# Optimization experiments

Measured on AMD Instinct MI355X. Metric: run time of the kernel, lower is better.

## Reference

```python
import jax, jax.numpy as jnp
import numpy as np

N_NODES = 100000
N_EDGES = 1600000
D_IN = 128
D_HID = 128


def setup_inputs() -> dict:
    key = jax.random.key(0)
    ks = jax.random.split(key, 8)
    scale_in = 1.0 / np.sqrt(D_IN)
    scale_h = 1.0 / np.sqrt(D_HID)
    return {
        "x": jax.random.normal(ks[0], (N_NODES, D_IN), dtype=jnp.float32),
        "edge_index": jax.random.randint(ks[1], (2, N_EDGES), 0, N_NODES, dtype=jnp.int64),
        "W_l1": jax.random.normal(ks[2], (D_IN, D_HID), dtype=jnp.float32) * scale_in,
        "W_r1": jax.random.normal(ks[3], (D_IN, D_HID), dtype=jnp.float32) * scale_in,
        "b1": jnp.zeros((D_HID,), dtype=jnp.float32),
        "W_l2": jax.random.normal(ks[4], (D_HID, D_HID), dtype=jnp.float32) * scale_h,
        "W_r2": jax.random.normal(ks[5], (D_HID, D_HID), dtype=jnp.float32) * scale_h,
        "b2": jnp.zeros((D_HID,), dtype=jnp.float32),
    }


def _sage_conv(h, src, dst, n_nodes, W_l, W_r, b):
    # mean aggregation of source-node features onto destination nodes
    msg = h[src]                                         # [E, d] gather
    agg = jax.ops.segment_sum(msg, dst, num_segments=n_nodes)   # [N, d]
    cnt = jax.ops.segment_sum(jnp.ones((src.shape[0], 1), h.dtype), dst,
                              num_segments=n_nodes)      # [N, 1]
    mean = agg / jnp.maximum(cnt, 1.0)                   # zero where no in-edges
    return mean @ W_l + b + h @ W_r                      # lin_l(mean) + lin_r(x)


def reference(x, edge_index, W_l1, W_r1, b1, W_l2, W_r2, b2):
    src, dst = edge_index[0], edge_index[1]
    n = x.shape[0]
    h = jax.nn.relu(_sage_conv(x, src, dst, n, W_l1, W_r1, b1))
    # dropout is identity in eval mode
    return _sage_conv(h, src, dst, n, W_l2, W_r2, b2)
```

## Files before the change

### kernel.cpp

```cpp
#include <hip/hip_runtime.h>
#include <stdint.h>

#define N_NODES 100000
#define N_EDGES 1600000
#define D 128
#define NBUCK 196
#define BSTRIDE 9216
#define PCHUNK 4096
#define NTILES (N_NODES / 16)
#define GRID_AG 2048

typedef unsigned int uint32;
typedef __attribute__((ext_vector_type(8))) short short8;
typedef __attribute__((ext_vector_type(4))) float f32x4;

__device__ __forceinline__ unsigned short f2bf(float f) {
  unsigned u = __builtin_bit_cast(unsigned, f);
  u += 0x7fffu + ((u >> 16) & 1u);
  return (unsigned short)(u >> 16);
}
__device__ __forceinline__ float bflo(unsigned v) {
  return __builtin_bit_cast(float, v << 16);
}
__device__ __forceinline__ float bfhi(unsigned v) {
  return __builtin_bit_cast(float, v & 0xffff0000u);
}


__global__ void k_zero(int* __restrict__ p, int n) {
  int i = blockIdx.x * blockDim.x + threadIdx.x;
  if (i < n) p[i] = 0;
}

__global__ __launch_bounds__(256) void k_part(const int* __restrict__ src,
                                              const int* __restrict__ dst,
                                              int* __restrict__ bcnt,
                                              uint2* __restrict__ pairs) {
  __shared__ uint2 buff[PCHUNK];
  __shared__ uint2 sorted[PCHUNK];
  __shared__ int hist[256], stmp[256], loff[256], cpos[256], base[256];
  int tid = threadIdx.x;
  int e0 = blockIdx.x * PCHUNK;
  int nv = N_EDGES - e0;
  if (nv > PCHUNK) nv = PCHUNK;

  hist[tid] = 0;
  __syncthreads();
  for (int i = tid; i < nv; i += 256) {
    int d = dst[e0 + i];
    int s = src[e0 + i];
    buff[i] = make_uint2((uint32)d, (uint32)s);
    atomicAdd(&hist[d >> 9], 1);
  }
  __syncthreads();
  int v = hist[tid];
  stmp[tid] = v;
  __syncthreads();
  for (int off = 1; off < 256; off <<= 1) {
    int t = (tid >= off) ? stmp[tid - off] : 0;
    __syncthreads();
    stmp[tid] += t;
    __syncthreads();
  }
  loff[tid] = stmp[tid] - v;
  cpos[tid] = stmp[tid] - v;
  base[tid] = (v > 0) ? atomicAdd(&bcnt[tid], v) : 0;
  __syncthreads();
  for (int i = tid; i < nv; i += 256) {
    uint2 p = buff[i];
    int r = atomicAdd(&cpos[p.x >> 9], 1);
    sorted[r] = p;
  }
  __syncthreads();
  for (int i = tid; i < nv; i += 256) {
    uint2 p = sorted[i];
    int b = (int)(p.x >> 9);
    int local = base[b] + (i - loff[b]);
    if (local < BSTRIDE)
      pairs[(size_t)b * BSTRIDE + local] = p;
  }
}

__global__ void k_scanb(const int* __restrict__ bcnt, int* __restrict__ bbase) {
  __shared__ int s[256];
  int tid = threadIdx.x;
  int v = (tid < NBUCK) ? bcnt[tid] : 0;
  s[tid] = v;
  __syncthreads();
  for (int off = 1; off < 256; off <<= 1) {
    int t = (tid >= off) ? s[tid - off] : 0;
    __syncthreads();
    s[tid] += t;
    __syncthreads();
  }
  if (tid <= NBUCK) bbase[tid] = s[tid] - v;
}

__global__ __launch_bounds__(512) void k_csr(const uint2* __restrict__ pairs,
                                             const int* __restrict__ bcnt,
                                             const int* __restrict__ bbase,
                                             int* __restrict__ rowptr,
                                             int* __restrict__ csr) {
  __shared__ int hist[512], off[512], cur[512];
  int b = blockIdx.x;
  int tid = threadIdx.x;
  int lo = b << 9;
  int hi = lo + 512;
  if (hi > N_NODES) hi = N_NODES;
  int ne = bcnt[b];
  if (ne > BSTRIDE) ne = BSTRIDE;
  const uint2* pb = pairs + (size_t)b * BSTRIDE;
  int bb = bbase[b];

  hist[tid] = 0;
  __syncthreads();
  for (int i = tid; i < ne; i += 512) atomicAdd(&hist[(int)pb[i].x - lo], 1);
  __syncthreads();
  int v = hist[tid];
  off[tid] = v;
  __syncthreads();
  for (int o = 1; o < 512; o <<= 1) {
    int t = (tid >= o) ? off[tid - o] : 0;
    __syncthreads();
    off[tid] += t;
    __syncthreads();
  }
  off[tid] -= v;
  cur[tid] = off[tid];
  if (lo + tid < hi) rowptr[lo + tid] = bb + off[tid];
  if (b == NBUCK - 1 && tid == 0) rowptr[N_NODES] = bbase[NBUCK];
  __syncthreads();
  for (int i = tid; i < ne; i += 512) {
    int d = (int)pb[i].x - lo;
    int slot = atomicAdd(&cur[d], 1);
    csr[bb + slot] = (int)pb[i].y;
  }
}


__global__ void k_cast(const float* __restrict__ in, unsigned short* __restrict__ ob, int n8) {
  int i = blockIdx.x * blockDim.x + threadIdx.x;
  if (i >= n8) return;
  float4 a = *reinterpret_cast<const float4*>(in + (size_t)i * 8);
  float4 b = *reinterpret_cast<const float4*>(in + (size_t)i * 8 + 4);
  uint4 o;
  o.x = (uint32)f2bf(a.x) | ((uint32)f2bf(a.y) << 16);
  o.y = (uint32)f2bf(a.z) | ((uint32)f2bf(a.w) << 16);
  o.z = (uint32)f2bf(b.x) | ((uint32)f2bf(b.y) << 16);
  o.w = (uint32)f2bf(b.z) | ((uint32)f2bf(b.w) << 16);
  *reinterpret_cast<uint4*>(ob + (size_t)i * 8) = o;
}

__global__ void k_prepw(const float* __restrict__ Wl, const float* __restrict__ Wr,
                        unsigned short* __restrict__ Wp) {
  int t = blockIdx.x * 256 + threadIdx.x;
  if (t >= 256 * 128) return;
  int j = t & 7;
  int lane = (t >> 3) & 63;
  int tile = (t >> 9) & 1;
  int ks = (t >> 10) & 7;
  int ng = (t >> 13) & 3;
  int k = ks * 32 + (lane >> 4) * 8 + j;
  int n = ng * 32 + tile * 16 + (lane & 15);
  float w = (k < 128) ? Wl[k * 128 + n] : Wr[(k - 128) * 128 + n];
  Wp[t] = f2bf(w);
}

__global__ __launch_bounds__(256) void k_agg_gemm(
    const unsigned short* __restrict__ table,
    const int* __restrict__ rowptr, const int* __restrict__ csr,
    const unsigned short* __restrict__ Wp, const float* __restrict__ bias,
    void* __restrict__ outp, int relu_bf16_out) {
  __shared__ float meanS[16][132];
  int tid = threadIdx.x;
  int wave = tid >> 6;
  int lane = tid & 63;
  int q = lane >> 4;
  int r = lane & 15;
  int g = tid >> 4;
  int l = tid & 15;

  short8 Bf[8][2];
  const unsigned short* wp = Wp + ((size_t)wave * 8 * 2) * 64 * 8 + lane * 8;
#pragma unroll
  for (int ks = 0; ks < 8; ++ks)
#pragma unroll
    for (int t = 0; t < 2; ++t)
      Bf[ks][t] = *reinterpret_cast<const short8*>(wp + (ks * 2 + t) * 512);

  float bia0 = bias[wave * 32 + r];
  float bia1 = bias[wave * 32 + 16 + r];

  for (int tile = blockIdx.x; tile < NTILES; tile += GRID_AG) {
    int node = tile * 16 + g;
    int beg = rowptr[node], end = rowptr[node + 1];
    float acc[8] = {0.f, 0.f, 0.f, 0.f, 0.f, 0.f, 0.f, 0.f};
    int e = beg;
    for (; e + 1 < end; e += 2) {
      int s0 = csr[e], s1 = csr[e + 1];
      uint4 v0 = *reinterpret_cast<const uint4*>(table + (size_t)s0 * D + l * 8);
      uint4 v1 = *reinterpret_cast<const uint4*>(table + (size_t)s1 * D + l * 8);
      acc[0] += bflo(v0.x); acc[1] += bfhi(v0.x);
      acc[2] += bflo(v0.y); acc[3] += bfhi(v0.y);
      acc[4] += bflo(v0.z); acc[5] += bfhi(v0.z);
      acc[6] += bflo(v0.w); acc[7] += bfhi(v0.w);
      acc[0] += bflo(v1.x); acc[1] += bfhi(v1.x);
      acc[2] += bflo(v1.y); acc[3] += bfhi(v1.y);
      acc[4] += bflo(v1.z); acc[5] += bfhi(v1.z);
      acc[6] += bflo(v1.w); acc[7] += bfhi(v1.w);
    }
    if (e < end) {
      int s0 = csr[e];
      uint4 v0 = *reinterpret_cast<const uint4*>(table + (size_t)s0 * D + l * 8);
      acc[0] += bflo(v0.x); acc[1] += bfhi(v0.x);
      acc[2] += bflo(v0.y); acc[3] += bfhi(v0.y);
      acc[4] += bflo(v0.z); acc[5] += bfhi(v0.z);
      acc[6] += bflo(v0.w); acc[7] += bfhi(v0.w);
    }
    float inv = (end > beg) ? 1.0f / (float)(end - beg) : 0.0f;
    float4 m0 = make_float4(acc[0] * inv, acc[1] * inv, acc[2] * inv, acc[3] * inv);
    float4 m1 = make_float4(acc[4] * inv, acc[5] * inv, acc[6] * inv, acc[7] * inv);
    *reinterpret_cast<float4*>(&meanS[g][l * 8]) = m0;
    *reinterpret_cast<float4*>(&meanS[g][l * 8 + 4]) = m1;
    __syncthreads();

    short8 A[8];
#pragma unroll
    for (int ks = 0; ks < 4; ++ks) {
      float4 a0 = *reinterpret_cast<const float4*>(&meanS[r][ks * 32 + q * 8]);
      float4 a1 = *reinterpret_cast<const float4*>(&meanS[r][ks * 32 + q * 8 + 4]);
      short8 a;
      a[0] = (short)f2bf(a0.x); a[1] = (short)f2bf(a0.y);
      a[2] = (short)f2bf(a0.z); a[3] = (short)f2bf(a0.w);
      a[4] = (short)f2bf(a1.x); a[5] = (short)f2bf(a1.y);
      a[6] = (short)f2bf(a1.z); a[7] = (short)f2bf(a1.w);
      A[ks] = a;
    }
    const unsigned short* ax = table + (size_t)(tile * 16 + r) * D + q * 8;
#pragma unroll
    for (int ks = 0; ks < 4; ++ks)
      A[4 + ks] = *reinterpret_cast<const short8*>(ax + ks * 32);

    f32x4 c0 = {0.f, 0.f, 0.f, 0.f}, c1 = {0.f, 0.f, 0.f, 0.f};
#pragma unroll
    for (int ks = 0; ks < 8; ++ks) {
      c0 = __builtin_amdgcn_mfma_f32_16x16x32_bf16(A[ks], Bf[ks][0], c0, 0, 0, 0);
      c1 = __builtin_amdgcn_mfma_f32_16x16x32_bf16(A[ks], Bf[ks][1], c1, 0, 0, 0);
    }

    int orow = tile * 16 + q * 4;
    if (relu_bf16_out) {
      unsigned short* ob = (unsigned short*)outp + (size_t)orow * D + wave * 32 + r;
#pragma unroll
      for (int gg = 0; gg < 4; ++gg) {
        ob[(size_t)gg * D] = f2bf(fmaxf(c0[gg] + bia0, 0.f));
        ob[(size_t)gg * D + 16] = f2bf(fmaxf(c1[gg] + bia1, 0.f));
      }
    } else {
      float* of = (float*)outp + (size_t)orow * D + wave * 32 + r;
#pragma unroll
      for (int gg = 0; gg < 4; ++gg) {
        of[(size_t)gg * D] = c0[gg] + bia0;
        of[(size_t)gg * D + 16] = c1[gg] + bia1;
      }
    }
    __syncthreads();
  }
}


extern "C" void kernel_launch(void* const* d_in, const int* in_sizes, int n_in,
                              void* d_out, int out_size, void* d_ws, size_t ws_size,
                              hipStream_t stream) {
  const float* x   = (const float*)d_in[0];
  const int*   ei  = (const int*)d_in[1];
  const float* Wl1 = (const float*)d_in[2];
  const float* Wr1 = (const float*)d_in[3];
  const float* b1  = (const float*)d_in[4];
  const float* Wl2 = (const float*)d_in[5];
  const float* Wr2 = (const float*)d_in[6];
  const float* b2  = (const float*)d_in[7];
  float* out = (float*)d_out;

  const int* esrc = ei;
  const int* edst = ei + N_EDGES;

  char* p = (char*)d_ws;
  auto take = [&](size_t bytes) {
    char* q = p;
    p += (bytes + 255) & ~(size_t)255;
    return q;
  };
  int* bcnt   = (int*)take(256 * 4);
  int* bbase  = (int*)take(257 * 4);
  int* rowptr = (int*)take((size_t)(N_NODES + 1) * 4);
  int* csr    = (int*)take((size_t)N_EDGES * 4);
  uint2* pairs = (uint2*)take((size_t)NBUCK * BSTRIDE * 8);
  unsigned short* xb  = (unsigned short*)take((size_t)N_NODES * D * 2);
  unsigned short* hb  = (unsigned short*)take((size_t)N_NODES * D * 2);
  unsigned short* Wp1 = (unsigned short*)take(256 * 128 * 2);
  unsigned short* Wp2 = (unsigned short*)take(256 * 128 * 2);

  const int npart = (N_EDGES + PCHUNK - 1) / PCHUNK;

  k_zero<<<1, 256, 0, stream>>>(bcnt, 256);
  k_part<<<npart, 256, 0, stream>>>(esrc, edst, bcnt, pairs);
  k_scanb<<<1, 256, 0, stream>>>(bcnt, bbase);
  k_csr<<<NBUCK, 512, 0, stream>>>(pairs, bcnt, bbase, rowptr, csr);

  k_cast<<<(N_NODES * D / 8 + 255) / 256, 256, 0, stream>>>(x, xb, N_NODES * D / 8);
  k_prepw<<<128, 256, 0, stream>>>(Wl1, Wr1, Wp1);
  k_prepw<<<128, 256, 0, stream>>>(Wl2, Wr2, Wp2);

  k_agg_gemm<<<GRID_AG, 256, 0, stream>>>(xb, rowptr, csr, Wp1, b1, hb, 1);
  k_agg_gemm<<<GRID_AG, 256, 0, stream>>>(hb, rowptr, csr, Wp2, b2, out, 0);
}
```

Baseline: 331.7 us.

## Merge weight prep kernels, unroll gather by four, hoist self-row loads

Several small changes at once. The two weight-packing launches become one kernel, and the zero kernel is replaced by hipMemsetAsync, cutting launch overhead. The neighbor gather loop is unrolled by four to keep more loads in flight. The self-feature A-fragment loads are hoisted ahead of the aggregation so their latency overlaps it. The partition chunk size is halved, which doubles the number of partition blocks.

```diff
diff --git a/kernel.cpp b/kernel.cpp
--- a/kernel.cpp
+++ b/kernel.cpp
@@ -6,7 +6,7 @@
 #define D 128
 #define NBUCK 196
 #define BSTRIDE 9216
-#define PCHUNK 4096
+#define PCHUNK 2048
 #define NTILES (N_NODES / 16)
 #define GRID_AG 2048
 
@@ -26,11 +26,6 @@
   return __builtin_bit_cast(float, v & 0xffff0000u);
 }
 
-
-__global__ void k_zero(int* __restrict__ p, int n) {
-  int i = blockIdx.x * blockDim.x + threadIdx.x;
-  if (i < n) p[i] = 0;
-}
 
 __global__ __launch_bounds__(256) void k_part(const int* __restrict__ src,
                                               const int* __restrict__ dst,
@@ -151,20 +146,31 @@
   *reinterpret_cast<uint4*>(ob + (size_t)i * 8) = o;
 }
 
-__global__ void k_prepw(const float* __restrict__ Wl, const float* __restrict__ Wr,
-                        unsigned short* __restrict__ Wp) {
+__global__ void k_prepw2(const float* __restrict__ Wl1, const float* __restrict__ Wr1,
+                         const float* __restrict__ Wl2, const float* __restrict__ Wr2,
+                         unsigned short* __restrict__ Wp1,
+                         unsigned short* __restrict__ Wp2) {
   int t = blockIdx.x * 256 + threadIdx.x;
-  if (t >= 256 * 128) return;
-  int j = t & 7;
-  int lane = (t >> 3) & 63;
-  int tile = (t >> 9) & 1;
-  int ks = (t >> 10) & 7;
-  int ng = (t >> 13) & 3;
+  int which = t >> 15;
+  int tt = t & 32767;
+  int j = tt & 7;
+  int lane = (tt >> 3) & 63;
+  int tile = (tt >> 9) & 1;
+  int ks = (tt >> 10) & 7;
+  int ng = (tt >> 13) & 3;
   int k = ks * 32 + (lane >> 4) * 8 + j;
   int n = ng * 32 + tile * 16 + (lane & 15);
+  const float* Wl = which ? Wl2 : Wl1;
+  const float* Wr = which ? Wr2 : Wr1;
   float w = (k < 128) ? Wl[k * 128 + n] : Wr[(k - 128) * 128 + n];
-  Wp[t] = f2bf(w);
-}
+  (which ? Wp2 : Wp1)[tt] = f2bf(w);
+}
+
+#define ACC8(v)                                          \
+  acc[0] += bflo(v.x); acc[1] += bfhi(v.x);              \
+  acc[2] += bflo(v.y); acc[3] += bfhi(v.y);              \
+  acc[4] += bflo(v.z); acc[5] += bfhi(v.z);              \
+  acc[6] += bflo(v.w); acc[7] += bfhi(v.w);
 
 __global__ __launch_bounds__(256) void k_agg_gemm(
     const unsigned short* __restrict__ table,
@@ -192,30 +198,28 @@
   float bia1 = bias[wave * 32 + 16 + r];
 
   for (int tile = blockIdx.x; tile < NTILES; tile += GRID_AG) {
+    const unsigned short* ax = table + (size_t)(tile * 16 + r) * D + q * 8;
+    short8 A[8];
+#pragma unroll
+    for (int ks = 0; ks < 4; ++ks)
+      A[4 + ks] = *reinterpret_cast<const short8*>(ax + ks * 32);
+
     int node = tile * 16 + g;
     int beg = rowptr[node], end = rowptr[node + 1];
     float acc[8] = {0.f, 0.f, 0.f, 0.f, 0.f, 0.f, 0.f, 0.f};
     int e = beg;
-    for (; e + 1 < end; e += 2) {
-      int s0 = csr[e], s1 = csr[e + 1];
+    for (; e + 3 < end; e += 4) {
+      int s0 = csr[e], s1 = csr[e + 1], s2 = csr[e + 2], s3 = csr[e + 3];
       uint4 v0 = *reinterpret_cast<const uint4*>(table + (size_t)s0 * D + l * 8);
       uint4 v1 = *reinterpret_cast<const uint4*>(table + (size_t)s1 * D + l * 8);
-      acc[0] += bflo(v0.x); acc[1] += bfhi(v0.x);
-      acc[2] += bflo(v0.y); acc[3] += bfhi(v0.y);
-      acc[4] += bflo(v0.z); acc[5] += bfhi(v0.z);
-      acc[6] += bflo(v0.w); acc[7] += bfhi(v0.w);
-      acc[0] += bflo(v1.x); acc[1] += bfhi(v1.x);
-      acc[2] += bflo(v1.y); acc[3] += bfhi(v1.y);
-      acc[4] += bflo(v1.z); acc[5] += bfhi(v1.z);
-      acc[6] += bflo(v1.w); acc[7] += bfhi(v1.w);
-    }
-    if (e < end) {
+      uint4 v2 = *reinterpret_cast<const uint4*>(table + (size_t)s2 * D + l * 8);
+      uint4 v3 = *reinterpret_cast<const uint4*>(table + (size_t)s3 * D + l * 8);
+      ACC8(v0) ACC8(v1) ACC8(v2) ACC8(v3)
+    }
+    for (; e < end; ++e) {
       int s0 = csr[e];
       uint4 v0 = *reinterpret_cast<const uint4*>(table + (size_t)s0 * D + l * 8);
-      acc[0] += bflo(v0.x); acc[1] += bfhi(v0.x);
-      acc[2] += bflo(v0.y); acc[3] += bfhi(v0.y);
-      acc[4] += bflo(v0.z); acc[5] += bfhi(v0.z);
-      acc[6] += bflo(v0.w); acc[7] += bfhi(v0.w);
+      ACC8(v0)
     }
     float inv = (end > beg) ? 1.0f / (float)(end - beg) : 0.0f;
     float4 m0 = make_float4(acc[0] * inv, acc[1] * inv, acc[2] * inv, acc[3] * inv);
@@ -224,7 +228,6 @@
     *reinterpret_cast<float4*>(&meanS[g][l * 8 + 4]) = m1;
     __syncthreads();
 
-    short8 A[8];
 #pragma unroll
     for (int ks = 0; ks < 4; ++ks) {
       float4 a0 = *reinterpret_cast<const float4*>(&meanS[r][ks * 32 + q * 8]);
@@ -236,10 +239,6 @@
       a[6] = (short)f2bf(a1.z); a[7] = (short)f2bf(a1.w);
       A[ks] = a;
     }
-    const unsigned short* ax = table + (size_t)(tile * 16 + r) * D + q * 8;
-#pragma unroll
-    for (int ks = 0; ks < 4; ++ks)
-      A[4 + ks] = *reinterpret_cast<const short8*>(ax + ks * 32);
 
     f32x4 c0 = {0.f, 0.f, 0.f, 0.f}, c1 = {0.f, 0.f, 0.f, 0.f};
 #pragma unroll
@@ -303,14 +302,13 @@
 
   const int npart = (N_EDGES + PCHUNK - 1) / PCHUNK;
 
-  k_zero<<<1, 256, 0, stream>>>(bcnt, 256);
+  hipMemsetAsync(bcnt, 0, 256 * 4, stream);
   k_part<<<npart, 256, 0, stream>>>(esrc, edst, bcnt, pairs);
   k_scanb<<<1, 256, 0, stream>>>(bcnt, bbase);
   k_csr<<<NBUCK, 512, 0, stream>>>(pairs, bcnt, bbase, rowptr, csr);
 
   k_cast<<<(N_NODES * D / 8 + 255) / 256, 256, 0, stream>>>(x, xb, N_NODES * D / 8);
-  k_prepw<<<128, 256, 0, stream>>>(Wl1, Wr1, Wp1);
-  k_prepw<<<128, 256, 0, stream>>>(Wl2, Wr2, Wp2);
+  k_prepw2<<<256, 256, 0, stream>>>(Wl1, Wr1, Wl2, Wr2, Wp1, Wp2);
 
   k_agg_gemm<<<GRID_AG, 256, 0, stream>>>(xb, rowptr, csr, Wp1, b1, hb, 1);
   k_agg_gemm<<<GRID_AG, 256, 0, stream>>>(hb, rowptr, csr, Wp2, b2, out, 0);
```

Result: no change. 330.3 us (-0.4%).
